# Performance work log

Hardware: AMD Instinct MI355X
Metric: run time of the kernel (lower is better)

Reference implementation:

```python
import jax, jax.numpy as jnp
import numpy as np

N_NODES = 100000
N_EDGES = 3200000
IN_FEATS = 512
HIDDEN = 64
N_CLASSES = 32


def setup_inputs() -> dict:
    key = jax.random.key(0)
    k1, k2, k3, k4 = jax.random.split(key, 4)
    x = jax.random.normal(k1, (N_NODES, IN_FEATS), dtype=jnp.float32)
    edge_index = jax.random.randint(k2, (2, N_EDGES), 0, N_NODES, dtype=jnp.int64)
    # Glorot-ish init for weights
    W1 = jax.random.normal(k3, (IN_FEATS, HIDDEN), dtype=jnp.float32) / np.sqrt(IN_FEATS)
    b1 = jnp.zeros((HIDDEN,), dtype=jnp.float32)
    W2 = jax.random.normal(k4, (HIDDEN, N_CLASSES), dtype=jnp.float32) / np.sqrt(HIDDEN)
    b2 = jnp.zeros((N_CLASSES,), dtype=jnp.float32)
    return {"x": x, "edge_index": edge_index, "W1": W1, "b1": b1, "W2": W2, "b2": b2}


def reference(x, edge_index, W1, b1, W2, b2):
    N = x.shape[0]
    # GCNConv default: add self-loops, unit edge weights (edge_attr is None for Cora)
    loop = jnp.arange(N, dtype=edge_index.dtype)
    src = jnp.concatenate([edge_index[0], loop])  # [E+N]
    dst = jnp.concatenate([edge_index[1], loop])  # [E+N]
    w = jnp.ones(src.shape[0], dtype=x.dtype)
    # symmetric normalization: deg^-1/2[src] * w * deg^-1/2[dst]
    deg = jax.ops.segment_sum(w, dst, num_segments=N)
    dinv = jnp.where(deg > 0, jax.lax.rsqrt(deg), 0.0)
    norm = dinv[src] * w * dinv[dst]  # [E+N]

    def gcn_layer(h, W, b):
        h = h @ W                              # transform first (out dim small)
        msg = h[src] * norm[:, None]           # gather + scale  [E+N, d_out]
        agg = jax.ops.segment_sum(msg, dst, num_segments=N)  # scatter-add
        return agg + b

    h = jax.nn.relu(gcn_layer(x, W1, b1))
    # F.dropout(training=self.training) -> identity in eval mode
    out = gcn_layer(h, W2, b2)
    return jax.nn.log_softmax(out, axis=1)
```

## Files before the change

kernel.cpp:

```cpp
#include <hip/hip_runtime.h>
#include <hip/hip_fp16.h>
#include <math.h>

constexpr int N_NODES = 100000;
constexpr int N_EDGES = 3200000;
constexpr int IN_F = 512;
constexpr int HID = 64;
constexpr int NCLS = 32;
constexpr int CAP = 80;
constexpr int SHIFT = 9;
constexpr int NB = 196;
constexpr int BCAPC = 16976;
constexpr int CHUNK = 8192;
constexpr int SENT = N_NODES;

constexpr int GEMM1_BLOCKS = (N_NODES + 63) / 64;
constexpr int PART_BLOCKS  = (N_EDGES + CHUNK - 1) / CHUNK;

typedef short short8 __attribute__((ext_vector_type(8)));
typedef float f32x4 __attribute__((ext_vector_type(4)));
typedef int intx4 __attribute__((ext_vector_type(4)));

__device__ __forceinline__ unsigned short f2bf(float f) {
    union { float f; unsigned int u; } v; v.f = f;
    unsigned int r = (v.u + 0x7fffu + ((v.u >> 16) & 1u)) >> 16;
    return (unsigned short)r;
}
__device__ __forceinline__ float bf2f(unsigned short h) {
    union { unsigned int u; float f; } v; v.u = ((unsigned int)h) << 16;
    return v.f;
}
__device__ __forceinline__ unsigned char f2e5(float f) {
    unsigned short u = __half_as_ushort(__float2half(f));
    return (unsigned char)((u + 0x7Fu + ((u >> 8) & 1u)) >> 8);
}
__device__ __forceinline__ float e52f(unsigned char b) {
    return __half2float(__ushort_as_half((unsigned short)((unsigned short)b << 8)));
}
__device__ __forceinline__ void gload16(const void* g, void* l) {
    __builtin_amdgcn_global_load_lds((const __attribute__((address_space(1))) unsigned int*)g,
                                     (__attribute__((address_space(3))) unsigned int*)l,
                                     16, 0, 0);
}

__global__ __launch_bounds__(256) void k_prep(const float* __restrict__ W1,
                                              unsigned short* __restrict__ W1T,
                                              unsigned char* __restrict__ h1s,
                                              unsigned char* __restrict__ h2s,
                                              int* __restrict__ gtail) {
    if (blockIdx.x == 128) {
        int t = threadIdx.x;
        if (t < HID)  h1s[(size_t)SENT * HID + t] = 0;
        if (t < NCLS) h2s[(size_t)SENT * NCLS + t] = 0;
        for (int i = t; i < NB * 16; i += 256) gtail[i] = 0;
        return;
    }
    int t = blockIdx.x * 256 + threadIdx.x;
    int k = t >> 6, c = t & 63;
    W1T[(size_t)c * IN_F + k] = f2bf(W1[(size_t)k * HID + c]);
}


__global__ __launch_bounds__(512) void k_part(const int* __restrict__ src,
                                              const int* __restrict__ dst,
                                              int* __restrict__ gtail,
                                              int* __restrict__ recs) {
    __shared__ alignas(16) char smem[47168];
    int* buf            = (int*)smem;
    unsigned char* bbuf = (unsigned char*)(smem + 32768);
    int* loc   = (int*)(smem + 40960);
    int* lh    = (int*)(smem + 43012);
    int* lbase = (int*)(smem + 45060);
    int* wsum  = (int*)(smem + 47108);
    const int tid = threadIdx.x;
    const int lane = tid & 63;
    const int wv = tid >> 6;
    const int c0 = blockIdx.x * CHUNK;
    const int cnum = min(CHUNK, N_EDGES - c0);
    lh[tid] = 0;
    __syncthreads();
    int dd[16], ss[16], rk[16];
    #pragma unroll
    for (int k = 0; k < 16; ++k) {
        int i = k * 512 + tid;
        if (i < cnum) {
            dd[k] = dst[c0 + i];
            ss[k] = src[c0 + i];
            rk[k] = atomicAdd(&lh[dd[k] >> SHIFT], 1);
        }
    }
    __syncthreads();
    int orig = lh[tid];
    int v = orig;
    #pragma unroll
    for (int off = 1; off < 64; off <<= 1) {
        int t = __shfl_up(v, off, 64);
        if (lane >= off) v += t;
    }
    if (lane == 63) wsum[wv] = v;
    __syncthreads();
    int pre = 0;
    #pragma unroll
    for (int k = 0; k < 8; ++k) if (k < wv) pre += wsum[k];
    int incl = v + pre;
    loc[tid] = incl - orig;
    if (tid < NB && orig > 0) lbase[tid] = atomicAdd(&gtail[tid * 16], orig);
    __syncthreads();
    #pragma unroll
    for (int k = 0; k < 16; ++k) {
        int i = k * 512 + tid;
        if (i < cnum) {
            int b = dd[k] >> SHIFT;
            int pos = loc[b] + rk[k];
            buf[pos] = ((dd[k] & 511) << 17) | ss[k];
            bbuf[pos] = (unsigned char)b;
        }
    }
    __syncthreads();
    for (int i = tid; i < cnum; i += 512) {
        int b = bbuf[i];
        int idx = lbase[b] + (i - loc[b]);
        if (idx < BCAPC) recs[(size_t)b * BCAPC + idx] = buf[i];
    }
}


__global__ __launch_bounds__(1024) void k_phase2(const int* __restrict__ gtail,
                                                 const int* __restrict__ recs,
                                                 int* __restrict__ slots,
                                                 int* __restrict__ cnt,
                                                 float* __restrict__ dinv) {
    __shared__ int scnt[512];
    const int b = blockIdx.x;
    const int tid = threadIdx.x;
    if (tid < 512) scnt[tid] = 0;
    __syncthreads();
    int nrec = min(gtail[b * 16], BCAPC);
    const int* rb = recs + (size_t)b * BCAPC;
    for (int i = tid; i < nrec; i += 1024) {
        int r = rb[i];
        int ln = r >> 17;
        int s  = r & 0x1FFFF;
        int p = atomicAdd(&scnt[ln], 1);
        int node = (b << SHIFT) + ln;
        if (p < CAP) slots[(size_t)node * CAP + p] = s;
    }
    __syncthreads();
    if (tid < 512) {
        int node = (b << SHIFT) + tid;
        if (node < N_NODES) {
            int c = scnt[tid];
            cnt[node] = c;
            dinv[node] = rsqrtf(1.0f + (float)c);
            int c2 = min(c, CAP);
            int degp = (c2 + 15) & ~15;
            for (int p = c2; p < degp; ++p) slots[(size_t)node * CAP + p] = SENT;
        }
    }
}


__global__ __launch_bounds__(256) void k_gemm1(const float* __restrict__ x,
                                               const unsigned short* __restrict__ W1T,
                                               const float* __restrict__ dinv,
                                               unsigned char* __restrict__ h1s) {
    __shared__ alignas(16) char smem[49152];
    float* Xf = (float*)smem;
    unsigned short* Wf = (unsigned short*)(smem + 32768);
    const int tid = threadIdx.x;
    const int lane = tid & 63;
    const int row0 = blockIdx.x * 64;
    const int w = tid >> 6;
    const int r0l = (w >> 1) * 32;
    const int c0l = (w & 1) * 32;
    const int lrow = lane & 15;
    const int lkb = (lane >> 4) << 3;
    f32x4 acc00 = {0.f, 0.f, 0.f, 0.f}, acc01 = acc00, acc10 = acc00, acc11 = acc00;

    const int rowA0 = tid >> 3;
    const int rowA1 = 32 + (tid >> 3);
    const int gA = tid & 7;
    const float* srcX0 = x + (size_t)min(row0 + rowA0, N_NODES - 1) * IN_F + ((gA ^ (rowA0 & 7)) << 2);
    const float* srcX1 = x + (size_t)min(row0 + rowA1, N_NODES - 1) * IN_F + ((gA ^ (rowA1 & 7)) << 2);
    const int rowW = tid >> 2;
    const int gW = tid & 3;
    const unsigned short* srcW = W1T + (size_t)rowW * IN_F + ((gW ^ (rowW & 3)) << 3);
    char* ldsX0 = smem + (w << 10);
    char* ldsX1 = smem + 4096 + (w << 10);
    char* ldsW  = smem + 32768 + (w << 10);

    #pragma unroll
    for (int s = 0; s < 3; ++s) {
        gload16(srcX0 + s * 32, ldsX0 + s * 8192);
        gload16(srcX1 + s * 32, ldsX1 + s * 8192);
        gload16(srcW  + s * 32, ldsW  + s * 4096);
    }

    const int RA = r0l + lrow, RA2 = RA + 16;
    const int RB = c0l + lrow, RB2 = RB + 16;
    const int qx = lkb >> 2;
    const int qw = lkb >> 3;
    const int sxA  = ((qx ^ (RA & 7)) << 2),  sxA_ = (((qx + 1) ^ (RA & 7)) << 2);
    const int sxB  = ((qx ^ (RA2 & 7)) << 2), sxB_ = (((qx + 1) ^ (RA2 & 7)) << 2);
    const int swB  = ((qw ^ (RB & 3)) << 3);
    const int swB2 = ((qw ^ (RB2 & 3)) << 3);

#define GEMM_COMPUTE(S)                                                          \
    {                                                                            \
        const int b_ = (S) & 3;                                                  \
        const float* xrA = Xf + b_ * 2048 + RA * 32;                             \
        const float* xrB = Xf + b_ * 2048 + RA2 * 32;                            \
        f32x4 va0 = *(const f32x4*)(xrA + sxA);                                  \
        f32x4 va1 = *(const f32x4*)(xrA + sxA_);                                 \
        f32x4 vb0 = *(const f32x4*)(xrB + sxB);                                  \
        f32x4 vb1 = *(const f32x4*)(xrB + sxB_);                                 \
        const unsigned short* wr = Wf + b_ * 2048;                               \
        short8 b0 = *(const short8*)(wr + RB * 32 + swB);                        \
        short8 b1 = *(const short8*)(wr + RB2 * 32 + swB2);                      \
        short8 a0, a1;                                                           \
        a0[0] = (short)f2bf(va0[0]); a0[1] = (short)f2bf(va0[1]);                \
        a0[2] = (short)f2bf(va0[2]); a0[3] = (short)f2bf(va0[3]);                \
        a0[4] = (short)f2bf(va1[0]); a0[5] = (short)f2bf(va1[1]);                \
        a0[6] = (short)f2bf(va1[2]); a0[7] = (short)f2bf(va1[3]);                \
        a1[0] = (short)f2bf(vb0[0]); a1[1] = (short)f2bf(vb0[1]);                \
        a1[2] = (short)f2bf(vb0[2]); a1[3] = (short)f2bf(vb0[3]);                \
        a1[4] = (short)f2bf(vb1[0]); a1[5] = (short)f2bf(vb1[1]);                \
        a1[6] = (short)f2bf(vb1[2]); a1[7] = (short)f2bf(vb1[3]);                \
        acc00 = __builtin_amdgcn_mfma_f32_16x16x32_bf16(a0, b0, acc00, 0, 0, 0); \
        acc01 = __builtin_amdgcn_mfma_f32_16x16x32_bf16(a0, b1, acc01, 0, 0, 0); \
        acc10 = __builtin_amdgcn_mfma_f32_16x16x32_bf16(a1, b0, acc10, 0, 0, 0); \
        acc11 = __builtin_amdgcn_mfma_f32_16x16x32_bf16(a1, b1, acc11, 0, 0, 0); \
    }

    for (int s = 0; s < 14; ++s) {
        asm volatile("s_waitcnt vmcnt(6)" ::: "memory");
        __builtin_amdgcn_s_barrier();
        __builtin_amdgcn_sched_barrier(0);
        if (s < 13) {
            gload16(srcX0 + (s + 3) * 32, ldsX0 + ((s + 3) & 3) * 8192);
            gload16(srcX1 + (s + 3) * 32, ldsX1 + ((s + 3) & 3) * 8192);
            gload16(srcW  + (s + 3) * 32, ldsW  + ((s + 3) & 3) * 4096);
        }
        GEMM_COMPUTE(s);
    }
    asm volatile("s_waitcnt vmcnt(3)" ::: "memory");
    __builtin_amdgcn_s_barrier();
    __builtin_amdgcn_sched_barrier(0);
    GEMM_COMPUTE(14);
    asm volatile("s_waitcnt vmcnt(0)" ::: "memory");
    __builtin_amdgcn_s_barrier();
    __builtin_amdgcn_sched_barrier(0);
    GEMM_COMPUTE(15);
#undef GEMM_COMPUTE

    const int vr0 = row0 + r0l + ((lane >> 4) << 2);
    const int gc0 = c0l + (lane & 15);
    #pragma unroll
    for (int v = 0; v < 4; ++v) {
        int gr = vr0 + v;
        if (gr < N_NODES) {
            float dv = dinv[gr];
            h1s[(size_t)gr * HID + gc0]      = f2e5(acc00[v] * dv);
            h1s[(size_t)gr * HID + gc0 + 16] = f2e5(acc01[v] * dv);
        }
        int gr2 = gr + 16;
        if (gr2 < N_NODES) {
            float dv2 = dinv[gr2];
            h1s[(size_t)gr2 * HID + gc0]      = f2e5(acc10[v] * dv2);
            h1s[(size_t)gr2 * HID + gc0 + 16] = f2e5(acc11[v] * dv2);
        }
    }
}


__global__ __launch_bounds__(256) void k_gather1(const int* __restrict__ cnt,
                                                 const int* __restrict__ slots,
                                                 const float* __restrict__ dinv,
                                                 const unsigned char* __restrict__ h1s,
                                                 const float* __restrict__ b1,
                                                 const float* __restrict__ W2,
                                                 unsigned char* __restrict__ h2s) {
    __shared__ alignas(16) float hsh[4][64];
    const int lane = threadIdx.x & 63;
    const int wv = threadIdx.x >> 6;
    const int cls = lane & 31;
    const int half = lane >> 5;
    float w[32];
    #pragma unroll
    for (int j = 0; j < 32; ++j)
        w[j] = W2[(size_t)(half * 32 + j) * NCLS + cls];
    const float bb = b1[lane];
    const int nw = gridDim.x * 4;
    for (int n0 = blockIdx.x * 4 + wv; n0 < N_NODES; n0 += nw) {
        const int n = __builtin_amdgcn_readfirstlane(n0);
        float dn = dinv[n];
        int deg = min(cnt[n], CAP);
        int degp = (deg + 15) & ~15;
        size_t base = (size_t)n * CAP;
        float a0 = e52f(h1s[(((unsigned)n) << 6) + lane]);
        float a1 = 0.f, a2 = 0.f, a3 = 0.f, a4 = 0.f, a5 = 0.f, a6 = 0.f, a7 = 0.f;
        for (int j = 0; j < degp; j += 16) {
            intx4 sa = *reinterpret_cast<const intx4*>(&slots[base + j]);
            intx4 sb = *reinterpret_cast<const intx4*>(&slots[base + j + 4]);
            intx4 sc = *reinterpret_cast<const intx4*>(&slots[base + j + 8]);
            intx4 sd = *reinterpret_cast<const intx4*>(&slots[base + j + 12]);
            a0 += e52f(h1s[(((unsigned)sa.x) << 6) + lane]);
            a1 += e52f(h1s[(((unsigned)sa.y) << 6) + lane]);
            a2 += e52f(h1s[(((unsigned)sa.z) << 6) + lane]);
            a3 += e52f(h1s[(((unsigned)sa.w) << 6) + lane]);
            a4 += e52f(h1s[(((unsigned)sb.x) << 6) + lane]);
            a5 += e52f(h1s[(((unsigned)sb.y) << 6) + lane]);
            a6 += e52f(h1s[(((unsigned)sb.z) << 6) + lane]);
            a7 += e52f(h1s[(((unsigned)sb.w) << 6) + lane]);
            a0 += e52f(h1s[(((unsigned)sc.x) << 6) + lane]);
            a1 += e52f(h1s[(((unsigned)sc.y) << 6) + lane]);
            a2 += e52f(h1s[(((unsigned)sc.z) << 6) + lane]);
            a3 += e52f(h1s[(((unsigned)sc.w) << 6) + lane]);
            a4 += e52f(h1s[(((unsigned)sd.x) << 6) + lane]);
            a5 += e52f(h1s[(((unsigned)sd.y) << 6) + lane]);
            a6 += e52f(h1s[(((unsigned)sd.z) << 6) + lane]);
            a7 += e52f(h1s[(((unsigned)sd.w) << 6) + lane]);
        }
        float v = fmaf(((a0 + a1) + (a2 + a3)) + ((a4 + a5) + (a6 + a7)), dn, bb);
        v = fmaxf(v, 0.f);
        hsh[wv][lane] = v;
        float acc = 0.f;
        #pragma unroll
        for (int q = 0; q < 8; ++q) {
            f32x4 hv = *reinterpret_cast<const f32x4*>(&hsh[wv][half * 32 + q * 4]);
            acc = fmaf(hv.x, w[q * 4 + 0], acc);
            acc = fmaf(hv.y, w[q * 4 + 1], acc);
            acc = fmaf(hv.z, w[q * 4 + 2], acc);
            acc = fmaf(hv.w, w[q * 4 + 3], acc);
        }
        acc += __shfl_xor(acc, 32, 64);
        if (half == 0)
            h2s[(((unsigned)n) << 5) + cls] = f2e5(acc * dn);
    }
}


__global__ __launch_bounds__(256) void k_out(const int* __restrict__ cnt,
                                             const int* __restrict__ slots,
                                             const float* __restrict__ dinv,
                                             const unsigned char* __restrict__ h2s,
                                             const float* __restrict__ b2,
                                             float* __restrict__ out) {
    int wid = blockIdx.x * 4 + (threadIdx.x >> 6);
    int n = __builtin_amdgcn_readfirstlane(wid);
    if (n >= N_NODES) return;
    int lane = threadIdx.x & 63;
    int cls = lane & 31;
    int half = lane >> 5;
    float dn = dinv[n];
    int deg = min(cnt[n], CAP);
    int degp = (deg + 15) & ~15;
    size_t base = (size_t)n * CAP;
    float a0 = half ? 0.f : e52f(h2s[(((unsigned)n) << 5) + cls]);
    float a1 = 0.f, a2 = 0.f, a3 = 0.f;
    for (int j = 0; j < degp; j += 16) {
        intx4 s0 = *reinterpret_cast<const intx4*>(&slots[base + j + half * 8]);
        intx4 s1 = *reinterpret_cast<const intx4*>(&slots[base + j + half * 8 + 4]);
        a0 += e52f(h2s[(((unsigned)s0.x) << 5) + cls]);
        a1 += e52f(h2s[(((unsigned)s0.y) << 5) + cls]);
        a2 += e52f(h2s[(((unsigned)s0.z) << 5) + cls]);
        a3 += e52f(h2s[(((unsigned)s0.w) << 5) + cls]);
        a0 += e52f(h2s[(((unsigned)s1.x) << 5) + cls]);
        a1 += e52f(h2s[(((unsigned)s1.y) << 5) + cls]);
        a2 += e52f(h2s[(((unsigned)s1.z) << 5) + cls]);
        a3 += e52f(h2s[(((unsigned)s1.w) << 5) + cls]);
    }
    float acc = (a0 + a1) + (a2 + a3);
    acc += __shfl_xor(acc, 32, 64);
    float z = fmaf(acc, dn, b2[cls]);
    float mx = z;
    #pragma unroll
    for (int d = 16; d > 0; d >>= 1) mx = fmaxf(mx, __shfl_xor(mx, d, 32));
    float ex = expf(z - mx);
    float sm = ex;
    #pragma unroll
    for (int d = 16; d > 0; d >>= 1) sm += __shfl_xor(sm, d, 32);
    if (half == 0)
        out[(size_t)n * NCLS + cls] = z - mx - logf(sm);
}


extern "C" void kernel_launch(void* const* d_in, const int* in_sizes, int n_in,
                              void* d_out, int out_size, void* d_ws, size_t ws_size,
                              hipStream_t stream) {
    const float* x  = (const float*)d_in[0];
    const int*   ei = (const int*)d_in[1];
    const float* W1 = (const float*)d_in[2];
    const float* b1 = (const float*)d_in[3];
    const float* W2 = (const float*)d_in[4];
    const float* b2 = (const float*)d_in[5];
    float* out = (float*)d_out;
    char* ws = (char*)d_ws;

    const int* src = ei;
    const int* dst = ei + N_EDGES;

    int*   gtail = (int*)ws;
    int*   cnt   = (int*)(ws + 16384);
    float* dinv  = (float*)(ws + 416384);
    unsigned short* W1T = (unsigned short*)(ws + 816384);
    int*   slots = (int*)(ws + 881920);
    unsigned char* h1s = (unsigned char*)(ws + 45682048ull);
    char*  recs_base   = ws + 52082176ull;
    int*   recs  = (int*)recs_base;
    unsigned char* h2s  = (unsigned char*)(ws + 65391360ull);

    k_prep<<<129, 256, 0, stream>>>(W1, W1T, h1s, h2s, gtail);
    k_part<<<PART_BLOCKS, 512, 0, stream>>>(src, dst, gtail, recs);
    k_phase2<<<NB, 1024, 0, stream>>>(gtail, recs, slots, cnt, dinv);
    k_gemm1<<<GEMM1_BLOCKS, 256, 0, stream>>>(x, W1T, dinv, h1s);
    k_gather1<<<1536, 256, 0, stream>>>(cnt, slots, dinv, h1s, b1, W2, h2s);
    k_out<<<(N_NODES + 3) / 4, 256, 0, stream>>>(cnt, slots, dinv, h2s, b2, out);
}
```

Before: 194.2 us.

## Split phase2 bucket fill across four blocks using global atomics

```diff
diff --git a/kernel.cpp b/kernel.cpp
--- a/kernel.cpp
+++ b/kernel.cpp
@@ -47,7 +47,10 @@
                                               unsigned short* __restrict__ W1T,
                                               unsigned char* __restrict__ h1s,
                                               unsigned char* __restrict__ h2s,
-                                              int* __restrict__ gtail) {
+                                              int* __restrict__ gtail,
+                                              int* __restrict__ cnt) {
+    for (int i = blockIdx.x * 256 + threadIdx.x; i < N_NODES; i += 129 * 256)
+        cnt[i] = 0;
     if (blockIdx.x == 128) {
         int t = threadIdx.x;
         if (t < HID)  h1s[(size_t)SENT * HID + t] = 0;
@@ -125,38 +128,38 @@
 }
 
 
-__global__ __launch_bounds__(1024) void k_phase2(const int* __restrict__ gtail,
-                                                 const int* __restrict__ recs,
-                                                 int* __restrict__ slots,
-                                                 int* __restrict__ cnt,
-                                                 float* __restrict__ dinv) {
-    __shared__ int scnt[512];
-    const int b = blockIdx.x;
-    const int tid = threadIdx.x;
-    if (tid < 512) scnt[tid] = 0;
-    __syncthreads();
+__global__ __launch_bounds__(512) void k_phase2(const int* __restrict__ gtail,
+                                                const int* __restrict__ recs,
+                                                int* __restrict__ slots,
+                                                int* __restrict__ cnt) {
+    const int b = blockIdx.x >> 2;
+    const int q = blockIdx.x & 3;
     int nrec = min(gtail[b * 16], BCAPC);
+    int n4 = (nrec + 3) >> 2;
+    int lo = q * n4;
+    int hi = min(nrec, lo + n4);
     const int* rb = recs + (size_t)b * BCAPC;
-    for (int i = tid; i < nrec; i += 1024) {
+    for (int i = lo + threadIdx.x; i < hi; i += 512) {
         int r = rb[i];
         int ln = r >> 17;
         int s  = r & 0x1FFFF;
-        int p = atomicAdd(&scnt[ln], 1);
         int node = (b << SHIFT) + ln;
+        int p = atomicAdd(&cnt[node], 1);
         if (p < CAP) slots[(size_t)node * CAP + p] = s;
     }
-    __syncthreads();
-    if (tid < 512) {
-        int node = (b << SHIFT) + tid;
-        if (node < N_NODES) {
-            int c = scnt[tid];
-            cnt[node] = c;
-            dinv[node] = rsqrtf(1.0f + (float)c);
-            int c2 = min(c, CAP);
-            int degp = (c2 + 15) & ~15;
-            for (int p = c2; p < degp; ++p) slots[(size_t)node * CAP + p] = SENT;
-        }
-    }
+}
+
+
+__global__ __launch_bounds__(512) void k_phase2b(int* __restrict__ slots,
+                                                 const int* __restrict__ cnt,
+                                                 float* __restrict__ dinv) {
+    int node = blockIdx.x * 512 + threadIdx.x;
+    if (node >= N_NODES) return;
+    int c = cnt[node];
+    dinv[node] = rsqrtf(1.0f + (float)c);
+    int c2 = min(c, CAP);
+    int degp = (c2 + 15) & ~15;
+    for (int p = c2; p < degp; ++p) slots[(size_t)node * CAP + p] = SENT;
 }
 
 
@@ -410,9 +413,10 @@
     int*   recs  = (int*)recs_base;
     unsigned char* h2s  = (unsigned char*)(ws + 65391360ull);
 
-    k_prep<<<129, 256, 0, stream>>>(W1, W1T, h1s, h2s, gtail);
+    k_prep<<<129, 256, 0, stream>>>(W1, W1T, h1s, h2s, gtail, cnt);
     k_part<<<PART_BLOCKS, 512, 0, stream>>>(src, dst, gtail, recs);
-    k_phase2<<<NB, 1024, 0, stream>>>(gtail, recs, slots, cnt, dinv);
+    k_phase2<<<NB * 4, 512, 0, stream>>>(gtail, recs, slots, cnt);
+    k_phase2b<<<(N_NODES + 511) / 512, 512, 0, stream>>>(slots, cnt, dinv);
     k_gemm1<<<GEMM1_BLOCKS, 256, 0, stream>>>(x, W1T, dinv, h1s);
     k_gather1<<<1536, 256, 0, stream>>>(cnt, slots, dinv, h1s, b1, W2, h2s);
     k_out<<<(N_NODES + 3) / 4, 256, 0, stream>>>(cnt, slots, dinv, h2s, b2, out);
```

New measurement: 265.8 us. 36.8% more time.
